# Performance work log

Hardware: AMD Instinct MI355X
Metric: run time of the kernel (lower is better)

The kernel has to match this reference:

```python
import jax, jax.numpy as jnp
import numpy as np

INPUT_DIM = 1024
HIDDEN_DIM = 2048
NUM_EMB = 4096
EMB_DIM = 256
N = 65536


def setup_inputs() -> dict:
    key = jax.random.key(0)
    ks = jax.random.split(key, 10)
    s = lambda fan_in: 1.0 / np.sqrt(fan_in)
    return {
        "x": jax.random.normal(ks[0], (N, INPUT_DIM), dtype=jnp.float32),
        # encoder: Linear(input_dim, hidden) -> ReLU -> Linear(hidden, emb)
        "W1": jax.random.uniform(ks[1], (INPUT_DIM, HIDDEN_DIM), jnp.float32, -s(INPUT_DIM), s(INPUT_DIM)),
        "b1": jax.random.uniform(ks[2], (HIDDEN_DIM,), jnp.float32, -s(INPUT_DIM), s(INPUT_DIM)),
        "W2": jax.random.uniform(ks[3], (HIDDEN_DIM, EMB_DIM), jnp.float32, -s(HIDDEN_DIM), s(HIDDEN_DIM)),
        "b2": jax.random.uniform(ks[4], (EMB_DIM,), jnp.float32, -s(HIDDEN_DIM), s(HIDDEN_DIM)),
        # codebook (nn.Embedding weight)
        "codebook": jax.random.normal(ks[5], (NUM_EMB, EMB_DIM), dtype=jnp.float32),
        # decoder: Linear(emb, hidden) -> ReLU -> Linear(hidden, input_dim)
        "W3": jax.random.uniform(ks[6], (EMB_DIM, HIDDEN_DIM), jnp.float32, -s(EMB_DIM), s(EMB_DIM)),
        "b3": jax.random.uniform(ks[7], (HIDDEN_DIM,), jnp.float32, -s(EMB_DIM), s(EMB_DIM)),
        "W4": jax.random.uniform(ks[8], (HIDDEN_DIM, INPUT_DIM), jnp.float32, -s(HIDDEN_DIM), s(HIDDEN_DIM)),
        "b4": jax.random.uniform(ks[9], (INPUT_DIM,), jnp.float32, -s(HIDDEN_DIM), s(HIDDEN_DIM)),
    }


def reference(x, W1, b1, W2, b2, codebook, W3, b3, W4, b4):
    # encoder
    h = jax.nn.relu(x @ W1 + b1)
    encoded = h @ W2 + b2                      # [N, E]
    # cdist (squared form; argmin is identical to Euclidean argmin)
    enc_sq = jnp.sum(encoded * encoded, axis=-1, keepdims=True)   # [N, 1]
    cb_sq = jnp.sum(codebook * codebook, axis=-1)                 # [K]
    d2 = enc_sq - 2.0 * (encoded @ codebook.T) + cb_sq            # [N, K]
    indices = jnp.argmin(d2, axis=-1)                             # [N]
    quantized = codebook[indices]                                 # [N, E]
    # decoder
    h2 = jax.nn.relu(quantized @ W3 + b3)
    decoded = h2 @ W4 + b4
    return (quantized, decoded)
```

## Files before the change

kernel.cpp:

```cpp
#include <hip/hip_runtime.h>

#define N_ROWS 65536
#define IN_DIM 1024
#define HID    2048
#define EMB    256
#define NCODE  4096

typedef __attribute__((ext_vector_type(8))) short bf16x8;
typedef __attribute__((ext_vector_type(4))) float f32x4;

__device__ __forceinline__ unsigned short f2bf(float v) {
    unsigned u = __float_as_uint(v);
    u += 0x7FFFu + ((u >> 16) & 1u);
    return (unsigned short)(u >> 16);
}
__device__ __forceinline__ float bf2f(unsigned short h) {
    return __uint_as_float(((unsigned)h) << 16);
}
__device__ __forceinline__ void gload16(const unsigned short* g, unsigned short* l) {
    __builtin_amdgcn_global_load_lds(
        (const __attribute__((address_space(1))) unsigned int*)g,
        (__attribute__((address_space(3))) unsigned int*)l, 16, 0, 0);
}

template<int SPLIT>
__global__ __launch_bounds__(256) void k_conv_w(
    const float* __restrict__ src, unsigned short* __restrict__ dh,
    unsigned short* __restrict__ dl, int NC, int nkt)
{
    const int t = threadIdx.x;
    const int nt = blockIdx.x, kt = blockIdx.y;
    const int kk = t >> 2, j4 = (t & 3) << 2;
    const int k0 = kt << 6, n0 = nt << 4;
    float4 v = *(const float4*)(src + (size_t)(k0 + kk) * NC + n0 + j4);
    size_t tb = ((size_t)nt * nkt + kt) * 1024 + ((kk >> 3) * 128) + (kk & 7);
    float vv[4] = {v.x, v.y, v.z, v.w};
    #pragma unroll
    for (int j = 0; j < 4; ++j) {
        unsigned short h = f2bf(vv[j]);
        dh[tb + (size_t)(j4 + j) * 8] = h;
        if (SPLIT) dl[tb + (size_t)(j4 + j) * 8] = f2bf(vv[j] - bf2f(h));
    }
}

__global__ __launch_bounds__(256) void k_conv_a(
    const float* __restrict__ src, unsigned short* __restrict__ dst, int Kw, int nkt)
{
    const int t = threadIdx.x;
    const int mt = blockIdx.x, kt = blockIdx.y;
    const int rr = t >> 4, k4 = (t & 15) << 2;
    float4 v = *(const float4*)(src + (size_t)(mt * 16 + rr) * Kw + kt * 64 + k4);
    size_t addr = ((size_t)mt * nkt + kt) * 1024 + (k4 >> 3) * 128 + rr * 8 + (k4 & 7);
    ushort4 h = { f2bf(v.x), f2bf(v.y), f2bf(v.z), f2bf(v.w) };
    *(ushort4*)&dst[addr] = h;
}

__global__ __launch_bounds__(256) void k_conv_cb(
    const float* __restrict__ cb, unsigned short* __restrict__ ch,
    unsigned short* __restrict__ cl_, float* __restrict__ halfsq)
{
    const int t = threadIdx.x;
    const int ct = blockIdx.x;
    const int cl = t >> 4, f = t & 15;
    const int code = (ct << 4) + cl;
    float ssq = 0.f;
    #pragma unroll
    for (int it = 0; it < 4; ++it) {
        const int k4 = (f << 2) + (it << 6);
        float4 v = *(const float4*)(cb + (size_t)code * EMB + k4);
        ssq += v.x * v.x + v.y * v.y + v.z * v.z + v.w * v.w;
        size_t tb = ((size_t)(ct * 4 + (k4 >> 6))) * 1024 + ((k4 >> 3) & 7) * 128 + cl * 8 + (k4 & 7);
        ushort4 h = { f2bf(v.x), f2bf(v.y), f2bf(v.z), f2bf(v.w) };
        *(ushort4*)&ch[tb] = h;
        ushort4 lo = { f2bf(v.x - bf2f(h.x)), f2bf(v.y - bf2f(h.y)),
                       f2bf(v.z - bf2f(h.z)), f2bf(v.w - bf2f(h.w)) };
        *(ushort4*)&cl_[tb] = lo;
    }
    #pragma unroll
    for (int off = 1; off <= 8; off <<= 1) ssq += __shfl_xor(ssq, off);
    if (f == 0) halfsq[code] = 0.5f * ssq;
}

template<int SPLIT, int AFMT, int OUTT>
__global__ __launch_bounds__(512, 2) void k_layer2(
    const float* __restrict__ A, const unsigned short* __restrict__ At,
    const unsigned short* __restrict__ Atl, int a_nkt,
    int lda, int K,
    const unsigned short* __restrict__ Bh, const unsigned short* __restrict__ Bl,
    int b_nkt, const float* __restrict__ bias, int biasoff,
    float* __restrict__ out, unsigned short* __restrict__ outt,
    unsigned short* __restrict__ outt2,
    int outw, int relu, int init, int ny_log2)
{
    constexpr int AL = 8192;
    constexpr int BH = SPLIT ? 16384 : 8192;
    __shared__ __align__(16) unsigned short s_mem[32768];

    const int t = threadIdx.x;
    const int id = blockIdx.x;
    const int m_low = id & 7, rest = id >> 3;
    const int nb = rest & ((1 << ny_log2) - 1);
    const int m0 = (((rest >> ny_log2) << 3) | m_low) * 128;
    const int nb0 = nb * 256;
    const int lane = t & 63, wv = t >> 6;
    const int wm = wv >> 2, wn = wv & 3;
    const int g = lane >> 4, rr = lane & 15;

    f32x4 acc[4][4];
    #pragma unroll
    for (int mi = 0; mi < 4; ++mi)
        #pragma unroll
        for (int ni = 0; ni < 4; ++ni) acc[mi][ni] = (f32x4){0.f, 0.f, 0.f, 0.f};

    for (int kc = 0; kc < K; kc += 64) {
        const int ktile = kc >> 6;
        #pragma unroll
        for (int jj = 0; jj < 2; ++jj) {
            const int j = wv * 2 + jj;
            const size_t gt = ((size_t)(nb0 / 16 + j) * b_nkt + ktile) * 1024;
            #pragma unroll
            for (int half = 0; half < 2; ++half)
                gload16(Bh + gt + half * 512 + lane * 8,
                        &s_mem[BH + j * 1024 + half * 512]);
        }
        if (AFMT == 0) {
            #pragma unroll
            for (int it = 0; it < 4; ++it) {
                int f = t + (it << 9);
                int r = f >> 4, k4 = (f & 15) << 2;
                float4 v = *(const float4*)(A + (size_t)(m0 + r) * lda + kc + k4);
                int mt = r >> 4, rl = r & 15, kb = k4 >> 3, e = k4 & 7;
                int addr = mt * 1024 + kb * 128 + ((rl ^ kb) << 3) + e;
                ushort4 hi, lo;
                hi.x = f2bf(v.x); hi.y = f2bf(v.y); hi.z = f2bf(v.z); hi.w = f2bf(v.w);
                *(ushort4*)&s_mem[addr] = hi;
                if (SPLIT) {
                    lo.x = f2bf(v.x - bf2f(hi.x)); lo.y = f2bf(v.y - bf2f(hi.y));
                    lo.z = f2bf(v.z - bf2f(hi.z)); lo.w = f2bf(v.w - bf2f(hi.w));
                    *(ushort4*)&s_mem[AL + addr] = lo;
                }
            }
        } else {
            const size_t gt = ((size_t)(m0 / 16 + wv) * a_nkt + ktile) * 1024;
            #pragma unroll
            for (int half = 0; half < 2; ++half)
                gload16(At + gt + half * 512 + lane * 8,
                        &s_mem[wv * 1024 + half * 512]);
            if (AFMT == 2) {
                #pragma unroll
                for (int half = 0; half < 2; ++half)
                    gload16(Atl + gt + half * 512 + lane * 8,
                            &s_mem[AL + wv * 1024 + half * 512]);
            }
        }
        __syncthreads();
        __builtin_amdgcn_s_setprio(1);
        #pragma unroll
        for (int s = 0; s < 2; ++s) {
            const int kb = (s << 2) + g;
            bf16x8 a_h[4], a_l[4], b_h[4], b_l[4];
            #pragma unroll
            for (int i = 0; i < 4; ++i) {
                int arow = (AFMT == 0) ? (((rr ^ kb) & 15) << 3) : (rr << 3);
                int aaddr = (wm * 4 + i) * 1024 + kb * 128 + arow;
                a_h[i] = *(const bf16x8*)&s_mem[aaddr];
                if (SPLIT) a_l[i] = *(const bf16x8*)&s_mem[AL + aaddr];
                int baddr = (wn * 4 + i) * 1024 + kb * 128 + (rr << 3);
                b_h[i] = *(const bf16x8*)&s_mem[BH + baddr];
                if (SPLIT)
                    b_l[i] = *(const bf16x8*)(Bl +
                        ((size_t)(nb0 / 16 + wn * 4 + i) * b_nkt + ktile) * 1024
                        + kb * 128 + (rr << 3));
            }
            #pragma unroll
            for (int mi = 0; mi < 4; ++mi)
                #pragma unroll
                for (int ni = 0; ni < 4; ++ni) {
                    acc[mi][ni] = __builtin_amdgcn_mfma_f32_16x16x32_bf16(a_h[mi], b_h[ni], acc[mi][ni], 0, 0, 0);
                    if (SPLIT) {
                        acc[mi][ni] = __builtin_amdgcn_mfma_f32_16x16x32_bf16(a_l[mi], b_h[ni], acc[mi][ni], 0, 0, 0);
                        acc[mi][ni] = __builtin_amdgcn_mfma_f32_16x16x32_bf16(a_h[mi], b_l[ni], acc[mi][ni], 0, 0, 0);
                    }
                }
        }
        __builtin_amdgcn_s_setprio(0);
        __syncthreads();
    }

    if (OUTT == 0) {
        float* sf = (float*)s_mem;
        for (int rm = 0; rm < 2; ++rm) {
            if (wm == rm) {
                #pragma unroll
                for (int mi = 0; mi < 4; ++mi)
                    #pragma unroll
                    for (int ni = 0; ni < 4; ++ni)
                        #pragma unroll
                        for (int rg = 0; rg < 4; ++rg)
                            sf[(mi * 16 + g * 4 + rg) * 256 + wn * 64 + ni * 16 + rr] = acc[mi][ni][rg];
            }
            __syncthreads();
            #pragma unroll
            for (int it = 0; it < 8; ++it) {
                int f = t + (it << 9);
                int r = f >> 6, c4 = (f & 63) << 2;
                float4 v = *(const float4*)&sf[r * 256 + c4];
                int gr = m0 + rm * 64 + r, gc = nb0 + c4;
                float* op = out + (size_t)gr * outw + gc;
                if (init) {
                    v.x += bias[biasoff + gc + 0]; v.y += bias[biasoff + gc + 1];
                    v.z += bias[biasoff + gc + 2]; v.w += bias[biasoff + gc + 3];
                } else {
                    float4 o = *(const float4*)op;
                    v.x += o.x; v.y += o.y; v.z += o.z; v.w += o.w;
                }
                if (relu) {
                    v.x = fmaxf(v.x, 0.f); v.y = fmaxf(v.y, 0.f);
                    v.z = fmaxf(v.z, 0.f); v.w = fmaxf(v.w, 0.f);
                }
                *(float4*)op = v;
            }
            __syncthreads();
        }
    } else {
        const int npass = (OUTT == 2) ? 2 : 1;
        for (int pass = 0; pass < npass; ++pass) {
            #pragma unroll
            for (int mi = 0; mi < 4; ++mi)
                #pragma unroll
                for (int ni = 0; ni < 4; ++ni) {
                    const int c = wn * 64 + ni * 16 + rr;
                    float bb = bias[biasoff + nb0 + c];
                    #pragma unroll
                    for (int rg = 0; rg < 4; ++rg) {
                        float v = acc[mi][ni][rg] + bb;
                        if (relu) v = fmaxf(v, 0.f);
                        unsigned short hi = f2bf(v);
                        unsigned short w = (pass == 0) ? hi : f2bf(v - bf2f(hi));
                        int addr = ((wm * 4 + mi) * 4 + wn) * 1024
                                 + (ni * 2 + (rr >> 3)) * 128 + (g * 4 + rg) * 8 + (rr & 7);
                        s_mem[addr] = w;
                    }
                }
            __syncthreads();
            unsigned short* dst = (pass == 0) ? outt : outt2;
            #pragma unroll
            for (int it = 0; it < 8; ++it) {
                int f = t + (it << 9);
                int tl = f >> 7, w8 = f & 127;
                size_t gaddr = ((size_t)(m0 / 16 + (tl >> 2)) * outw + nb0 / 64 + (tl & 3)) * 1024;
                *(float4*)(dst + gaddr + w8 * 8) = *(const float4*)&s_mem[tl * 1024 + w8 * 8];
            }
            __syncthreads();
        }
    }
}

__global__ __launch_bounds__(512, 2) void k_dist(
    float* encq, const unsigned short* __restrict__ ch,
    const unsigned short* __restrict__ cl,
    const float* __restrict__ hsq, const float* __restrict__ cb)
{
    __shared__ __align__(16) unsigned short s_cb[2][16384];
    __shared__ int s_c1[256], s_c2[256];

    const int t = threadIdx.x;
    const int lane = t & 63, wv = t >> 6;
    const int g = lane >> 4, rr = lane & 15;
    const int r0 = blockIdx.x * 256;

    bf16x8 eh[2][8], el[2][8];
    #pragma unroll
    for (int rg = 0; rg < 2; ++rg) {
        const float* ep = encq + (size_t)(r0 + wv * 32 + rg * 16 + rr) * EMB + g * 8;
        #pragma unroll
        for (int s = 0; s < 8; ++s) {
            float4 v0 = *(const float4*)(ep + s * 32);
            float4 v1 = *(const float4*)(ep + s * 32 + 4);
            float vv[8] = {v0.x, v0.y, v0.z, v0.w, v1.x, v1.y, v1.z, v1.w};
            bf16x8 a, b;
            #pragma unroll
            for (int j = 0; j < 8; ++j) {
                unsigned short h = f2bf(vv[j]);
                a[j] = (short)h;
                b[j] = (short)f2bf(vv[j] - bf2f(h));
            }
            eh[rg][s] = a; el[rg][s] = b;
        }
    }
    float b1v[2][4], b2v[2][4]; int i1v[2][4], i2v[2][4];
    #pragma unroll
    for (int rg = 0; rg < 2; ++rg)
        #pragma unroll
        for (int r2 = 0; r2 < 4; ++r2) {
            b1v[rg][r2] = -1e30f; b2v[rg][r2] = -1e30f;
            i1v[rg][r2] = 0; i2v[rg][r2] = 0;
        }

    #define STAGE(buf, c)                                                              \
        {                                                                              \
            const unsigned short* gh_ = ch + (size_t)(c) * 8192 + wv * 1024;           \
            const unsigned short* gl_ = cl + (size_t)(c) * 8192 + wv * 1024;           \
            _Pragma("unroll")                                                          \
            for (int i_ = 0; i_ < 2; ++i_) {                                           \
                gload16(gh_ + i_ * 512 + lane * 8, &s_cb[buf][wv * 1024 + i_ * 512]);  \
                gload16(gl_ + i_ * 512 + lane * 8, &s_cb[buf][8192 + wv * 1024 + i_ * 512]); \
            }                                                                          \
        }

    #define COMPUTE(cur, c, hv_)                                                       \
        {                                                                              \
            f32x4 ahh[2][2], ahl[2][2], alh[2][2];                                     \
            _Pragma("unroll")                                                          \
            for (int rg = 0; rg < 2; ++rg)                                             \
                _Pragma("unroll")                                                      \
                for (int ci = 0; ci < 2; ++ci) {                                       \
                    ahh[rg][ci] = (f32x4){0.f, 0.f, 0.f, 0.f};                         \
                    ahl[rg][ci] = (f32x4){0.f, 0.f, 0.f, 0.f};                         \
                    alh[rg][ci] = (f32x4){0.f, 0.f, 0.f, 0.f};                         \
                }                                                                      \
            __builtin_amdgcn_s_setprio(1);                                             \
            _Pragma("unroll")                                                          \
            for (int s = 0; s < 8; ++s) {                                              \
                const int ktile = s >> 1, kb = ((s & 1) << 2) + g;                     \
                _Pragma("unroll")                                                      \
                for (int ci = 0; ci < 2; ++ci) {                                       \
                    const int off = (ci * 4 + ktile) * 1024 + kb * 128 + rr * 8;       \
                    bf16x8 bh = *(const bf16x8*)&s_cb[cur][off];                       \
                    bf16x8 bl = *(const bf16x8*)&s_cb[cur][8192 + off];                \
                    _Pragma("unroll")                                                  \
                    for (int rg = 0; rg < 2; ++rg) {                                   \
                        ahh[rg][ci] = __builtin_amdgcn_mfma_f32_16x16x32_bf16(eh[rg][s], bh, ahh[rg][ci], 0, 0, 0); \
                        ahl[rg][ci] = __builtin_amdgcn_mfma_f32_16x16x32_bf16(eh[rg][s], bl, ahl[rg][ci], 0, 0, 0); \
                        alh[rg][ci] = __builtin_amdgcn_mfma_f32_16x16x32_bf16(el[rg][s], bh, alh[rg][ci], 0, 0, 0); \
                    }                                                                  \
                }                                                                      \
            }                                                                          \
            __builtin_amdgcn_s_setprio(0);                                             \
            _Pragma("unroll")                                                          \
            for (int rg = 0; rg < 2; ++rg)                                             \
                _Pragma("unroll")                                                      \
                for (int ci = 0; ci < 2; ++ci) {                                       \
                    f32x4 av = ahh[rg][ci] + ahl[rg][ci] + alh[rg][ci];                \
                    const int code = ((c) << 5) + (ci << 4) + rr;                      \
                    const float hs = __shfl(hv_, ci * 16 + rr);                        \
                    _Pragma("unroll")                                                  \
                    for (int r2 = 0; r2 < 4; ++r2) {                                   \
                        float v = av[r2] - hs;                                         \
                        bool bt1 = (v > b1v[rg][r2]) || (v == b1v[rg][r2] && code < i1v[rg][r2]); \
                        bool bt2 = (v > b2v[rg][r2]) || (v == b2v[rg][r2] && code < i2v[rg][r2]); \
                        if (bt1) { b2v[rg][r2] = b1v[rg][r2]; i2v[rg][r2] = i1v[rg][r2]; \
                                   b1v[rg][r2] = v; i1v[rg][r2] = code; }              \
                        else if (bt2) { b2v[rg][r2] = v; i2v[rg][r2] = code; }         \
                    }                                                                  \
                }                                                                      \
        }

    STAGE(0, 0)
    int cur = 0;
    for (int c = 0; c < 127; ++c) {
        STAGE(cur ^ 1, c + 1)
        float hv_ = hsq[(c << 5) + (lane & 31)];
        asm volatile("s_waitcnt vmcnt(5)" ::: "memory");
        __builtin_amdgcn_s_barrier();
        __builtin_amdgcn_sched_barrier(0);
        COMPUTE(cur, c, hv_)
        asm volatile("" ::: "memory");
        __builtin_amdgcn_s_barrier();
        cur ^= 1;
    }
    {
        float hv_ = hsq[(127 << 5) + (lane & 31)];
        asm volatile("s_waitcnt vmcnt(0)" ::: "memory");
        __builtin_amdgcn_s_barrier();
        __builtin_amdgcn_sched_barrier(0);
        COMPUTE(cur, 127, hv_)
    }
    #undef STAGE
    #undef COMPUTE

    #pragma unroll
    for (int off = 1; off <= 8; off <<= 1) {
        #pragma unroll
        for (int rg = 0; rg < 2; ++rg)
            #pragma unroll
            for (int r2 = 0; r2 < 4; ++r2) {
                float ob1 = __shfl_xor(b1v[rg][r2], off), ob2 = __shfl_xor(b2v[rg][r2], off);
                int oi1 = __shfl_xor(i1v[rg][r2], off), oi2 = __shfl_xor(i2v[rg][r2], off);
                bool ofirst = (ob1 > b1v[rg][r2]) || (ob1 == b1v[rg][r2] && oi1 < i1v[rg][r2]);
                if (ofirst) {
                    bool mysec = (b1v[rg][r2] > ob2) || (b1v[rg][r2] == ob2 && i1v[rg][r2] < oi2);
                    b2v[rg][r2] = mysec ? b1v[rg][r2] : ob2; i2v[rg][r2] = mysec ? i1v[rg][r2] : oi2;
                    b1v[rg][r2] = ob1; i1v[rg][r2] = oi1;
                } else {
                    bool osec = (ob1 > b2v[rg][r2]) || (ob1 == b2v[rg][r2] && oi1 < i2v[rg][r2]);
                    b2v[rg][r2] = osec ? ob1 : b2v[rg][r2]; i2v[rg][r2] = osec ? oi1 : i2v[rg][r2];
                }
            }
    }
    if (rr == 0) {
        #pragma unroll
        for (int rg = 0; rg < 2; ++rg)
            #pragma unroll
            for (int r2 = 0; r2 < 4; ++r2) {
                int rl = wv * 32 + rg * 16 + g * 4 + r2;
                s_c1[rl] = i1v[rg][r2]; s_c2[rl] = i2v[rg][r2];
            }
    }
    __syncthreads();

    for (int rloc = 0; rloc < 32; ++rloc) {
        const int row = wv * 32 + rloc;
        const int c1 = s_c1[row], c2 = s_c2[row];
        float4 ev = *(const float4*)(encq + (size_t)(r0 + row) * EMB + lane * 4);
        float4 v1 = *(const float4*)(cb + (size_t)c1 * EMB + lane * 4);
        float4 v2 = *(const float4*)(cb + (size_t)c2 * EMB + lane * 4);
        float d1 = ev.x * v1.x + ev.y * v1.y + ev.z * v1.z + ev.w * v1.w;
        float d2 = ev.x * v2.x + ev.y * v2.y + ev.z * v2.z + ev.w * v2.w;
        #pragma unroll
        for (int off = 1; off <= 32; off <<= 1) {
            d1 += __shfl_xor(d1, off);
            d2 += __shfl_xor(d2, off);
        }
        if (lane == 0) {
            float s1 = d1 - hsq[c1], s2 = d2 - hsq[c2];
            bool keep1 = (s1 > s2) || (s1 == s2 && c1 < c2);
            s_c1[row] = keep1 ? c1 : c2;
        }
    }
    __syncthreads();
    #pragma unroll
    for (int it = 0; it < 32; ++it) {
        int f = t + (it << 9);
        int row = f >> 6, c4 = (f & 63) << 2;
        int bi = s_c1[row];
        *(float4*)(encq + (size_t)(r0 + row) * EMB + c4) =
            *(const float4*)(cb + (size_t)bi * EMB + c4);
    }
}

__global__ __launch_bounds__(256) void k_dec_fb(
    const float* __restrict__ qz,
    const float* __restrict__ W3, const float* __restrict__ b3,
    const float* __restrict__ W4, const float* __restrict__ b4,
    float* __restrict__ outd) {
    __shared__ float s_q[8][EMB];
    __shared__ float s_h2[8][HID];
    const int t = threadIdx.x;
    const int row0 = blockIdx.x * 8;
    #pragma unroll
    for (int r = 0; r < 8; ++r) s_q[r][t] = qz[(size_t)(row0 + r) * EMB + t];
    __syncthreads();
    for (int gg = 0; gg < 8; ++gg) {
        const int j = (gg << 8) + t;
        float acc[8];
        #pragma unroll
        for (int r = 0; r < 8; ++r) acc[r] = 0.f;
        const float* wp = W3 + j;
        for (int e = 0; e < EMB; e += 4) {
            const float w0 = wp[(size_t)(e + 0) * HID];
            const float w1v = wp[(size_t)(e + 1) * HID];
            const float w2v = wp[(size_t)(e + 2) * HID];
            const float w3v = wp[(size_t)(e + 3) * HID];
            #pragma unroll
            for (int r = 0; r < 8; ++r) {
                const float4 qv = *reinterpret_cast<const float4*>(&s_q[r][e]);
                acc[r] = fmaf(qv.x, w0, acc[r]);
                acc[r] = fmaf(qv.y, w1v, acc[r]);
                acc[r] = fmaf(qv.z, w2v, acc[r]);
                acc[r] = fmaf(qv.w, w3v, acc[r]);
            }
        }
        const float bb = b3[j];
        #pragma unroll
        for (int r = 0; r < 8; ++r) s_h2[r][j] = fmaxf(acc[r] + bb, 0.f);
    }
    __syncthreads();
    float acc4[8][4];
    #pragma unroll
    for (int r = 0; r < 8; ++r)
        #pragma unroll
        for (int ci = 0; ci < 4; ++ci) acc4[r][ci] = 0.f;
    const float* w4p = W4 + t;
    for (int k = 0; k < HID; k += 4) {
        float wv[4][4];
        #pragma unroll
        for (int ki = 0; ki < 4; ++ki)
            #pragma unroll
            for (int ci = 0; ci < 4; ++ci)
                wv[ki][ci] = w4p[(size_t)(k + ki) * IN_DIM + (ci << 8)];
        #pragma unroll
        for (int r = 0; r < 8; ++r) {
            const float4 hv = *reinterpret_cast<const float4*>(&s_h2[r][k]);
            #pragma unroll
            for (int ci = 0; ci < 4; ++ci) {
                acc4[r][ci] = fmaf(hv.x, wv[0][ci], acc4[r][ci]);
                acc4[r][ci] = fmaf(hv.y, wv[1][ci], acc4[r][ci]);
                acc4[r][ci] = fmaf(hv.z, wv[2][ci], acc4[r][ci]);
                acc4[r][ci] = fmaf(hv.w, wv[3][ci], acc4[r][ci]);
            }
        }
    }
    #pragma unroll
    for (int ci = 0; ci < 4; ++ci) {
        const float bb = b4[(ci << 8) + t];
        #pragma unroll
        for (int r = 0; r < 8; ++r)
            outd[(size_t)(row0 + r) * IN_DIM + (ci << 8) + t] = acc4[r][ci] + bb;
    }
}

extern "C" void kernel_launch(void* const* d_in, const int* in_sizes, int n_in,
                              void* d_out, int out_size, void* d_ws, size_t ws_size,
                              hipStream_t stream) {
    const float* x  = (const float*)d_in[0];
    const float* W1 = (const float*)d_in[1];
    const float* b1 = (const float*)d_in[2];
    const float* W2 = (const float*)d_in[3];
    const float* b2 = (const float*)d_in[4];
    const float* cb = (const float*)d_in[5];
    const float* W3 = (const float*)d_in[6];
    const float* b3 = (const float*)d_in[7];
    const float* W4 = (const float*)d_in[8];
    const float* b4 = (const float*)d_in[9];

    float* outq = (float*)d_out;
    float* outd = outq + (size_t)N_ROWS * EMB;

    unsigned short* ou = (unsigned short*)outd;
    unsigned short* W1Th = ou;
    unsigned short* W1Tl = ou + 2097152;
    unsigned short* W2Th = ou + 4194304;
    unsigned short* W2Tl = ou + 4718592;
    unsigned short* cbh  = ou + 5242880;
    unsigned short* cbl  = ou + 6291456;
    float* halfsq = outd + 3670016;
    unsigned short* h_hi = (unsigned short*)(outd + 4194304);
    unsigned short* h_lo = h_hi + 33554432;
    unsigned short* qt = (unsigned short*)(outd + 58720256);
    float* enc = outq;

    const bool fastdec = ws_size >= (size_t)72351744;
    unsigned short* W3Th = (unsigned short*)d_ws;
    unsigned short* W4Th = W3Th + 524288;
    unsigned short* h2t  = (unsigned short*)((char*)d_ws + 5242880);

    k_conv_w<1><<<dim3(128, 16), 256, 0, stream>>>(W1, W1Th, W1Tl, HID, 16);
    k_conv_w<1><<<dim3(16, 32), 256, 0, stream>>>(W2, W2Th, W2Tl, EMB, 32);
    k_conv_cb<<<256, 256, 0, stream>>>(cb, cbh, cbl, halfsq);
    if (fastdec) {
        k_conv_w<0><<<dim3(128, 4), 256, 0, stream>>>(W3, W3Th, nullptr, HID, 4);
        k_conv_w<0><<<dim3(64, 32), 256, 0, stream>>>(W4, W4Th, nullptr, IN_DIM, 32);
    }
    for (int q = 0; q < 4; ++q) {
        k_layer2<1, 0, 2><<<1024, 512, 0, stream>>>(
            x, nullptr, nullptr, 0, IN_DIM, IN_DIM,
            W1Th + (size_t)q * 524288, W1Tl + (size_t)q * 524288, 16,
            b1, q * 512, nullptr, h_hi, h_lo, 8, 1, 0, 1);
        k_layer2<1, 2, 0><<<512, 512, 0, stream>>>(
            nullptr, h_hi, h_lo, 8, 0, 512,
            W2Th + (size_t)q * 8192, W2Tl + (size_t)q * 8192, 32,
            b2, 0, enc, nullptr, nullptr, EMB, 0, q == 0, 0);
    }
    k_dist<<<256, 512, 0, stream>>>(enc, cbh, cbl, halfsq, cb);
    if (fastdec) {
        k_conv_a<<<dim3(4096, 4), 256, 0, stream>>>(outq, qt, EMB, 4);
        for (int s = 0; s < 4; ++s) {
            const size_t roff = (size_t)s * 16384;
            k_layer2<0, 1, 1><<<1024, 512, 0, stream>>>(
                nullptr, qt + (size_t)s * 4194304, nullptr, 4, 0, EMB,
                W3Th, nullptr, 4,
                b3, 0, nullptr, h2t, nullptr, 32, 1, 0, 3);
            k_layer2<0, 1, 0><<<512, 512, 0, stream>>>(
                nullptr, h2t, nullptr, 32, 0, HID,
                W4Th, nullptr, 32,
                b4, 0, outd + roff * IN_DIM, nullptr, nullptr, IN_DIM, 0, 1, 2);
        }
    } else {
        k_dec_fb<<<N_ROWS / 8, 256, 0, stream>>>(outq, W3, b3, W4, b4, outd);
    }
}
```

Before: 2.436 ms.

## Double-buffer LDS tiles in layer GEMM to overlap loads with MFMA

Converts the single-buffered K loop of k_layer2 into a two-stage ping-pong pipeline. Global-to-LDS DMA and fp32 A register prefetch for the next k-tile are issued before the MFMA compute on the current tile, with one barrier per iteration instead of two. LDS use doubles, so launch bounds drop from 2 to 1 blocks per CU minimum, which may lower occupancy and latency hiding across blocks.

Measured after the change: 2.374 ms. 2.6% less time.

```diff
diff --git a/kernel.cpp b/kernel.cpp
--- a/kernel.cpp
+++ b/kernel.cpp
@@ -82,7 +82,7 @@
 }
 
 template<int SPLIT, int AFMT, int OUTT>
-__global__ __launch_bounds__(512, 2) void k_layer2(
+__global__ __launch_bounds__(512, 1) void k_layer2(
     const float* __restrict__ A, const unsigned short* __restrict__ At,
     const unsigned short* __restrict__ Atl, int a_nkt,
     int lda, int K,
@@ -92,9 +92,10 @@
     unsigned short* __restrict__ outt2,
     int outw, int relu, int init, int ny_log2)
 {
+    constexpr int BUFSZ = SPLIT ? 32768 : 24576;
     constexpr int AL = 8192;
     constexpr int BH = SPLIT ? 16384 : 8192;
-    __shared__ __align__(16) unsigned short s_mem[32768];
+    __shared__ __align__(16) unsigned short s_mem[2 * BUFSZ];
 
     const int t = threadIdx.x;
     const int id = blockIdx.x;
@@ -105,6 +106,7 @@
     const int lane = t & 63, wv = t >> 6;
     const int wm = wv >> 2, wn = wv & 3;
     const int g = lane >> 4, rr = lane & 15;
+    const int nt = K >> 6;
 
     f32x4 acc[4][4];
     #pragma unroll
@@ -112,80 +114,126 @@
         #pragma unroll
         for (int ni = 0; ni < 4; ++ni) acc[mi][ni] = (f32x4){0.f, 0.f, 0.f, 0.f};
 
-    for (int kc = 0; kc < K; kc += 64) {
-        const int ktile = kc >> 6;
-        #pragma unroll
-        for (int jj = 0; jj < 2; ++jj) {
-            const int j = wv * 2 + jj;
-            const size_t gt = ((size_t)(nb0 / 16 + j) * b_nkt + ktile) * 1024;
-            #pragma unroll
-            for (int half = 0; half < 2; ++half)
-                gload16(Bh + gt + half * 512 + lane * 8,
-                        &s_mem[BH + j * 1024 + half * 512]);
-        }
-        if (AFMT == 0) {
-            #pragma unroll
-            for (int it = 0; it < 4; ++it) {
-                int f = t + (it << 9);
-                int r = f >> 4, k4 = (f & 15) << 2;
-                float4 v = *(const float4*)(A + (size_t)(m0 + r) * lda + kc + k4);
-                int mt = r >> 4, rl = r & 15, kb = k4 >> 3, e = k4 & 7;
-                int addr = mt * 1024 + kb * 128 + ((rl ^ kb) << 3) + e;
-                ushort4 hi, lo;
-                hi.x = f2bf(v.x); hi.y = f2bf(v.y); hi.z = f2bf(v.z); hi.w = f2bf(v.w);
-                *(ushort4*)&s_mem[addr] = hi;
-                if (SPLIT) {
-                    lo.x = f2bf(v.x - bf2f(hi.x)); lo.y = f2bf(v.y - bf2f(hi.y));
-                    lo.z = f2bf(v.z - bf2f(hi.z)); lo.w = f2bf(v.w - bf2f(hi.w));
-                    *(ushort4*)&s_mem[AL + addr] = lo;
-                }
-            }
-        } else {
-            const size_t gt = ((size_t)(m0 / 16 + wv) * a_nkt + ktile) * 1024;
-            #pragma unroll
-            for (int half = 0; half < 2; ++half)
-                gload16(At + gt + half * 512 + lane * 8,
-                        &s_mem[wv * 1024 + half * 512]);
-            if (AFMT == 2) {
-                #pragma unroll
-                for (int half = 0; half < 2; ++half)
-                    gload16(Atl + gt + half * 512 + lane * 8,
-                            &s_mem[AL + wv * 1024 + half * 512]);
-            }
-        }
-        __syncthreads();
-        __builtin_amdgcn_s_setprio(1);
-        #pragma unroll
-        for (int s = 0; s < 2; ++s) {
-            const int kb = (s << 2) + g;
-            bf16x8 a_h[4], a_l[4], b_h[4], b_l[4];
-            #pragma unroll
-            for (int i = 0; i < 4; ++i) {
-                int arow = (AFMT == 0) ? (((rr ^ kb) & 15) << 3) : (rr << 3);
-                int aaddr = (wm * 4 + i) * 1024 + kb * 128 + arow;
-                a_h[i] = *(const bf16x8*)&s_mem[aaddr];
-                if (SPLIT) a_l[i] = *(const bf16x8*)&s_mem[AL + aaddr];
-                int baddr = (wn * 4 + i) * 1024 + kb * 128 + (rr << 3);
-                b_h[i] = *(const bf16x8*)&s_mem[BH + baddr];
-                if (SPLIT)
-                    b_l[i] = *(const bf16x8*)(Bl +
-                        ((size_t)(nb0 / 16 + wn * 4 + i) * b_nkt + ktile) * 1024
-                        + kb * 128 + (rr << 3));
-            }
-            #pragma unroll
-            for (int mi = 0; mi < 4; ++mi)
-                #pragma unroll
-                for (int ni = 0; ni < 4; ++ni) {
-                    acc[mi][ni] = __builtin_amdgcn_mfma_f32_16x16x32_bf16(a_h[mi], b_h[ni], acc[mi][ni], 0, 0, 0);
-                    if (SPLIT) {
-                        acc[mi][ni] = __builtin_amdgcn_mfma_f32_16x16x32_bf16(a_l[mi], b_h[ni], acc[mi][ni], 0, 0, 0);
-                        acc[mi][ni] = __builtin_amdgcn_mfma_f32_16x16x32_bf16(a_h[mi], b_l[ni], acc[mi][ni], 0, 0, 0);
-                    }
-                }
-        }
-        __builtin_amdgcn_s_setprio(0);
-        __syncthreads();
-    }
+    #define STAGE_DMA(buf, ktile)                                                      \
+        {                                                                              \
+            unsigned short* base_ = &s_mem[(buf) * BUFSZ];                             \
+            _Pragma("unroll")                                                          \
+            for (int jj = 0; jj < 2; ++jj) {                                           \
+                const int j_ = wv * 2 + jj;                                            \
+                const size_t gt_ = ((size_t)(nb0 / 16 + j_) * b_nkt + (ktile)) * 1024; \
+                _Pragma("unroll")                                                      \
+                for (int hf = 0; hf < 2; ++hf)                                         \
+                    gload16(Bh + gt_ + hf * 512 + lane * 8,                            \
+                            base_ + BH + j_ * 1024 + hf * 512);                        \
+            }                                                                          \
+            if (AFMT >= 1) {                                                           \
+                const size_t ga_ = ((size_t)(m0 / 16 + wv) * a_nkt + (ktile)) * 1024;  \
+                _Pragma("unroll")                                                      \
+                for (int hf = 0; hf < 2; ++hf)                                         \
+                    gload16(At + ga_ + hf * 512 + lane * 8,                            \
+                            base_ + wv * 1024 + hf * 512);                             \
+                if (AFMT == 2) {                                                       \
+                    _Pragma("unroll")                                                  \
+                    for (int hf = 0; hf < 2; ++hf)                                     \
+                        gload16(Atl + ga_ + hf * 512 + lane * 8,                       \
+                                base_ + AL + wv * 1024 + hf * 512);                    \
+                }                                                                      \
+            }                                                                          \
+        }
+
+    #define A_LOAD(ktile, pv)                                                          \
+        {                                                                              \
+            _Pragma("unroll")                                                          \
+            for (int it = 0; it < 4; ++it) {                                           \
+                int f_ = t + (it << 9);                                                \
+                int r_ = f_ >> 4, k4_ = (f_ & 15) << 2;                                \
+                pv[it] = *(const float4*)(A + (size_t)(m0 + r_) * lda + (ktile) * 64 + k4_); \
+            }                                                                          \
+        }
+
+    #define A_WRITE(buf, pv)                                                           \
+        {                                                                              \
+            unsigned short* base_ = &s_mem[(buf) * BUFSZ];                             \
+            _Pragma("unroll")                                                          \
+            for (int it = 0; it < 4; ++it) {                                           \
+                int f_ = t + (it << 9);                                                \
+                int r_ = f_ >> 4, k4_ = (f_ & 15) << 2;                                \
+                int mt_ = r_ >> 4, rl_ = r_ & 15, kb_ = k4_ >> 3, e_ = k4_ & 7;        \
+                int addr_ = mt_ * 1024 + kb_ * 128 + ((rl_ ^ kb_) << 3) + e_;          \
+                float4 v_ = pv[it];                                                    \
+                ushort4 hi_, lo_;                                                      \
+                hi_.x = f2bf(v_.x); hi_.y = f2bf(v_.y); hi_.z = f2bf(v_.z); hi_.w = f2bf(v_.w); \
+                *(ushort4*)&base_[addr_] = hi_;                                        \
+                if (SPLIT) {                                                           \
+                    lo_.x = f2bf(v_.x - bf2f(hi_.x)); lo_.y = f2bf(v_.y - bf2f(hi_.y)); \
+                    lo_.z = f2bf(v_.z - bf2f(hi_.z)); lo_.w = f2bf(v_.w - bf2f(hi_.w)); \
+                    *(ushort4*)&base_[AL + addr_] = lo_;                               \
+                }                                                                      \
+            }                                                                          \
+        }
+
+    #define COMPUTE(buf, ktile)                                                        \
+        {                                                                              \
+            const unsigned short* base_ = &s_mem[(buf) * BUFSZ];                       \
+            __builtin_amdgcn_s_setprio(1);                                             \
+            _Pragma("unroll")                                                          \
+            for (int s = 0; s < 2; ++s) {                                              \
+                const int kb = (s << 2) + g;                                           \
+                bf16x8 a_h[4], a_l[4], b_h[4], b_l[4];                                 \
+                _Pragma("unroll")                                                      \
+                for (int i = 0; i < 4; ++i) {                                          \
+                    int arow = (AFMT == 0) ? (((rr ^ kb) & 15) << 3) : (rr << 3);      \
+                    int aaddr = (wm * 4 + i) * 1024 + kb * 128 + arow;                 \
+                    a_h[i] = *(const bf16x8*)&base_[aaddr];                            \
+                    if (SPLIT) a_l[i] = *(const bf16x8*)&base_[AL + aaddr];            \
+                    int baddr = (wn * 4 + i) * 1024 + kb * 128 + (rr << 3);            \
+                    b_h[i] = *(const bf16x8*)&base_[BH + baddr];                       \
+                    if (SPLIT)                                                         \
+                        b_l[i] = *(const bf16x8*)(Bl +                                 \
+                            ((size_t)(nb0 / 16 + wn * 4 + i) * b_nkt + (ktile)) * 1024 \
+                            + kb * 128 + (rr << 3));                                   \
+                }                                                                      \
+                _Pragma("unroll")                                                      \
+                for (int mi = 0; mi < 4; ++mi)                                         \
+                    _Pragma("unroll")                                                  \
+                    for (int ni = 0; ni < 4; ++ni) {                                   \
+                        acc[mi][ni] = __builtin_amdgcn_mfma_f32_16x16x32_bf16(a_h[mi], b_h[ni], acc[mi][ni], 0, 0, 0); \
+                        if (SPLIT) {                                                   \
+                            acc[mi][ni] = __builtin_amdgcn_mfma_f32_16x16x32_bf16(a_l[mi], b_h[ni], acc[mi][ni], 0, 0, 0); \
+                            acc[mi][ni] = __builtin_amdgcn_mfma_f32_16x16x32_bf16(a_h[mi], b_l[ni], acc[mi][ni], 0, 0, 0); \
+                        }                                                              \
+                    }                                                                  \
+            }                                                                          \
+            __builtin_amdgcn_s_setprio(0);                                             \
+        }
+
+    float4 pv[4];
+    STAGE_DMA(0, 0)
+    if (AFMT == 0) {
+        A_LOAD(0, pv)
+        A_WRITE(0, pv)
+    }
+    asm volatile("s_waitcnt vmcnt(0) lgkmcnt(0)" ::: "memory");
+    __builtin_amdgcn_s_barrier();
+    __builtin_amdgcn_sched_barrier(0);
+
+    int cur = 0;
+    for (int kt = 0; kt < nt; ++kt) {
+        if (kt + 1 < nt) {
+            STAGE_DMA(cur ^ 1, kt + 1)
+            if (AFMT == 0) A_LOAD(kt + 1, pv)
+        }
+        COMPUTE(cur, kt)
+        if (AFMT == 0) { if (kt + 1 < nt) A_WRITE(cur ^ 1, pv) }
+        asm volatile("s_waitcnt vmcnt(0) lgkmcnt(0)" ::: "memory");
+        __builtin_amdgcn_s_barrier();
+        __builtin_amdgcn_sched_barrier(0);
+        cur ^= 1;
+    }
+    #undef STAGE_DMA
+    #undef A_LOAD
+    #undef A_WRITE
+    #undef COMPUTE
 
     if (OUTT == 0) {
         float* sf = (float*)s_mem;
```
